# Optimization experiments

Hardware: AMD Instinct MI355X
Metric: run time of the kernel (lower is better)

## Reference

```python
import jax, jax.numpy as jnp
import numpy as np

B, S, H, E, TOPK = 8, 512, 1024, 8, 2


def setup_inputs() -> dict:
    key = jax.random.key(0)
    ks = jax.random.split(key, 10)
    D = 2 * H
    inp = {
        "vector": jax.random.normal(ks[0], (B, S, D), dtype=jnp.float32),
        # gate weights (Linear(H, E)): stored as [H, E] for x @ W + b
        "Wg": jax.random.normal(ks[1], (H, E), dtype=jnp.float32) * 0.02,
        "bg": jnp.zeros((E,), dtype=jnp.float32),
        "Wf": jax.random.normal(ks[2], (H, E), dtype=jnp.float32) * 0.02,
        "bf": jnp.zeros((E,), dtype=jnp.float32),
        # expert MLP weights, stacked over experts: Linear(2H,2H) -> ReLU -> Linear(2H,2H)
        "W1": jax.random.normal(ks[3], (E, D, D), dtype=jnp.float32) * 0.02,
        "b1": jnp.zeros((E, D), dtype=jnp.float32),
        "W2": jax.random.normal(ks[4], (E, D, D), dtype=jnp.float32) * 0.02,
        "b2": jnp.zeros((E, D), dtype=jnp.float32),
        # combine weights (config['initializer_weight'])
        "weight": jnp.ones((2,), dtype=jnp.float32),
        "top_k": TOPK,
    }
    return inp


def reference(vector, Wg, bg, Wf, bf, W1, b1, W2, b2, weight, top_k):
    h = Wg.shape[0]
    n_exp = Wg.shape[1]
    # gate_g on first half, softmax, then top-k sparsify (scatter of topk values)
    rout_g = jax.nn.softmax(vector[:, :, :h] @ Wg + bg, axis=-1)           # [B,S,E]
    vals, idx = jax.lax.top_k(rout_g, top_k)                               # [B,S,k]
    route_g = jnp.sum(jax.nn.one_hot(idx, n_exp, dtype=vals.dtype) * vals[..., None], axis=-2)  # [B,S,E]
    # gate_f on second half: dense softmax routing
    rout_f = jax.nn.softmax(vector[:, :, h:2 * h] @ Wf + bf, axis=-1)      # [B,S,E]
    # dense expert computation for every token (dropout = identity at eval)
    hidden = jax.nn.relu(jnp.einsum('bsd,edh->bseh', vector, W1) + b1)     # [B,S,E,2H]
    expert_out = jnp.einsum('bseh,ehd->bsed', hidden, W2) + b2             # [B,S,E,2H]
    out0 = weight[0] * jnp.einsum('bsed,bse->bsd', expert_out[..., :h], route_g)
    out1 = weight[1] * jnp.einsum('bsed,bse->bsd', expert_out[..., h:2 * h], rout_f)
    return (out0, out1)
```

## Files before the change

### kernel.cpp

```cpp
#include <hip/hip_runtime.h>

#define TOKENS 4096
#define DDIM   2048
#define HDIM   1024
#define NEXP   8
#define GK     2048
#define GN     2048

typedef __bf16 bf16_t;
typedef __bf16 bf16x8 __attribute__((ext_vector_type(8)));
typedef __bf16 bf16x4 __attribute__((ext_vector_type(4)));
typedef float  f32x4  __attribute__((ext_vector_type(4)));

__device__ inline void gld_lds16(const bf16_t* g, bf16_t* l) {
  __builtin_amdgcn_global_load_lds(
      (const __attribute__((address_space(1))) void*)g,
      (__attribute__((address_space(3))) void*)l, 16, 0, 0);
}

#define LGKM0() asm volatile("s_waitcnt lgkmcnt(0)" ::: "memory")
#define VMC(n)  asm volatile("s_waitcnt vmcnt(" #n ")" ::: "memory")
#define BAR()   __builtin_amdgcn_s_barrier()

__global__ __launch_bounds__(256)
void k_routing(const float* __restrict__ vec,
               const float* __restrict__ Wg, const float* __restrict__ bg,
               const float* __restrict__ Wf, const float* __restrict__ bfv,
               const float* __restrict__ wgt,
               float* __restrict__ c0, float* __restrict__ c1)
{
  const int wave = threadIdx.x >> 6;
  const int lane = threadIdx.x & 63;
  const int m = blockIdx.x * 4 + wave;
  const float* v = vec + (size_t)m * DDIM;

  float ag[NEXP], af[NEXP];
#pragma unroll
  for (int e = 0; e < NEXP; ++e) { ag[e] = 0.f; af[e] = 0.f; }

  for (int i = lane; i < HDIM; i += 64) {
    const float xg = v[i];
    const float xf = v[HDIM + i];
    const float4 wg0 = *(const float4*)(Wg + i * NEXP);
    const float4 wg1 = *(const float4*)(Wg + i * NEXP + 4);
    const float4 wf0 = *(const float4*)(Wf + i * NEXP);
    const float4 wf1 = *(const float4*)(Wf + i * NEXP + 4);
    ag[0] += xg * wg0.x; ag[1] += xg * wg0.y; ag[2] += xg * wg0.z; ag[3] += xg * wg0.w;
    ag[4] += xg * wg1.x; ag[5] += xg * wg1.y; ag[6] += xg * wg1.z; ag[7] += xg * wg1.w;
    af[0] += xf * wf0.x; af[1] += xf * wf0.y; af[2] += xf * wf0.z; af[3] += xf * wf0.w;
    af[4] += xf * wf1.x; af[5] += xf * wf1.y; af[6] += xf * wf1.z; af[7] += xf * wf1.w;
  }
#pragma unroll
  for (int e = 0; e < NEXP; ++e) {
#pragma unroll
    for (int off = 32; off >= 1; off >>= 1) {
      ag[e] += __shfl_xor(ag[e], off, 64);
      af[e] += __shfl_xor(af[e], off, 64);
    }
  }
  if (lane == 0) {
    float g[NEXP], f[NEXP];
    float mg = -1e30f, mf = -1e30f;
#pragma unroll
    for (int e = 0; e < NEXP; ++e) {
      g[e] = ag[e] + bg[e]; mg = fmaxf(mg, g[e]);
      f[e] = af[e] + bfv[e]; mf = fmaxf(mf, f[e]);
    }
    float sg = 0.f, sf = 0.f;
#pragma unroll
    for (int e = 0; e < NEXP; ++e) {
      g[e] = expf(g[e] - mg); sg += g[e];
      f[e] = expf(f[e] - mf); sf += f[e];
    }
    const float rg = 1.f / sg, rf = 1.f / sf;
#pragma unroll
    for (int e = 0; e < NEXP; ++e) { g[e] *= rg; f[e] *= rf; }
    int i1 = 0;
#pragma unroll
    for (int e = 1; e < NEXP; ++e) if (g[e] > g[i1]) i1 = e;
    int i2 = (i1 == 0) ? 1 : 0;
#pragma unroll
    for (int e = 0; e < NEXP; ++e) if (e != i1 && g[e] > g[i2]) i2 = e;
    const float w0 = wgt[0], w1 = wgt[1];
#pragma unroll
    for (int e = 0; e < NEXP; ++e) {
      c0[e * TOKENS + m] = (e == i1 || e == i2) ? w0 * g[e] : 0.f;
      c1[e * TOKENS + m] = w1 * f[e];
    }
  }
}

__global__ __launch_bounds__(256)
void k_cvt(const float* __restrict__ in, bf16_t* __restrict__ out)
{
  const size_t i = ((size_t)blockIdx.x * 256 + threadIdx.x) * 8;
  const float4 a = *(const float4*)(in + i);
  const float4 b = *(const float4*)(in + i + 4);
  bf16x8 o;
  o[0] = (bf16_t)a.x; o[1] = (bf16_t)a.y; o[2] = (bf16_t)a.z; o[3] = (bf16_t)a.w;
  o[4] = (bf16_t)b.x; o[5] = (bf16_t)b.y; o[6] = (bf16_t)b.z; o[7] = (bf16_t)b.w;
  *(bf16x8*)(out + i) = o;
}

#define TP 68
__global__ __launch_bounds__(256)
void k_cvt_wt(const float* __restrict__ W, bf16_t* __restrict__ Wt)
{
  __shared__ __attribute__((aligned(16))) bf16_t tile[64 * TP];
  const size_t eoff = (size_t)blockIdx.z * DDIM * DDIM;
  const float* w = W + eoff;
  bf16_t* wt = Wt + eoff;
  const int k0 = blockIdx.x * 64;
  const int n0 = blockIdx.y * 64;
  const int t = threadIdx.x;
  const int c4 = (t & 15) * 4;
  const int rb = (t >> 4) * 4;
#pragma unroll
  for (int rr = 0; rr < 4; ++rr) {
    const int r = rb + rr;
    const float4 v = *(const float4*)(w + (size_t)(k0 + r) * DDIM + n0 + c4);
    tile[(c4 + 0) * TP + r] = (bf16_t)v.x;
    tile[(c4 + 1) * TP + r] = (bf16_t)v.y;
    tile[(c4 + 2) * TP + r] = (bf16_t)v.z;
    tile[(c4 + 3) * TP + r] = (bf16_t)v.w;
  }
  __syncthreads();
  const int nl = t >> 2;
  const int kq = (t & 3) * 16;
  bf16_t* dst = wt + (size_t)(n0 + nl) * DDIM + k0 + kq;
#pragma unroll
  for (int j2 = 0; j2 < 4; ++j2) {
    bf16x4 u = *(const bf16x4*)(&tile[nl * TP + kq + j2 * 4]);
    *(bf16x4*)(dst + j2 * 4) = u;
  }
}


#define FRG(base, R, KQ) \
  (*(const bf16x8*)((base) + ((((R) * 32 + (KQ)) ^ ((((R) >> 3) & 1) << 4)))))

#define MFMA_(d, x, y) (d) = __builtin_amdgcn_mfma_f32_16x16x32_bf16((x), (y), (d), 0, 0, 0)

#define PHASE(U, PA, STA, STB, NP) do { \
    bf16x8 _a[8], _b0, _b1; \
    _Pragma("unroll") \
    for (int _i = 0; _i < 8; ++_i) _a[_i] = FRG(AsF + (U) * 8192, wm + _i * 16 + fr, kq); \
    _b0 = FRG(BsF + (U) * 4096, wn + fr, kq); \
    _b1 = FRG(BsF + (U) * 4096, wn + 16 + fr, kq); \
    if ((PA) < (NP)) { STA(PA, (PA) & 3); STB(PA, (PA) & 3); } \
    BAR(); LGKM0(); \
    __builtin_amdgcn_s_setprio(1); \
    _Pragma("unroll") \
    for (int _i = 0; _i < 8; ++_i) { MFMA_(acc[_i][0], _a[_i], _b0); MFMA_(acc[_i][1], _a[_i], _b1); } \
    __builtin_amdgcn_s_setprio(0); \
  } while (0)

#define TILE(U0, U1, PA, PB, STA, STB, NP) do { \
    PHASE(U0, PA, STA, STB, NP); \
    BAR(); \
    PHASE(U1, PB, STA, STB, NP); \
    if ((PB) < (NP)) { VMC(3); } else { VMC(0); } \
    BAR(); \
  } while (0)

__global__ __launch_bounds__(512, 2)
void k_gemm1_8p(const bf16_t* __restrict__ A, const bf16_t* __restrict__ W1t,
                const float* __restrict__ b1, bf16_t* __restrict__ Hd)
{
  __shared__ __attribute__((aligned(16))) bf16_t AsF[4 * 8192];
  __shared__ __attribute__((aligned(16))) bf16_t BsF[4 * 4096];
  const int e = blockIdx.z;
  const int t = threadIdx.x;
  const int wave = t >> 6, lane = t & 63;
  const int m0 = blockIdx.x * 256, n0 = blockIdx.y * 128;
  const int wm = (wave >> 2) * 128, wn = (wave & 3) * 32;
  const int fr = lane & 15, kq = (lane >> 4) * 8;

  const int sRw = wave * 16 + (lane >> 2);
  const int sC  = ((lane & 3) * 8) ^ (((lane >> 5) & 1) << 4);
  const bf16_t* aSrc = A + (size_t)(m0 + sRw) * GK + sC;
  const bf16_t* bSrc = W1t + (size_t)e * GN * GK + (size_t)(n0 + sRw) * GK + sC;
  bf16_t* aDst = AsF + wave * 512;
  bf16_t* bDst = BsF + wave * 512;

#define STA1(p, u) do { const bf16_t* _s = aSrc + (size_t)(p) * 32; \
    gld_lds16(_s, aDst + (u) * 8192); \
    gld_lds16(_s + (size_t)128 * GK, aDst + (u) * 8192 + 4096); } while (0)
#define STB1(p, u) gld_lds16(bSrc + (size_t)(p) * 32, bDst + (u) * 4096)

  f32x4 acc[8][2] = {};

  STA1(0, 0); STB1(0, 0);
  STA1(1, 1); STB1(1, 1);
  STA1(2, 2); STB1(2, 2);
  asm volatile("s_waitcnt vmcnt(3)" ::: "memory");
  BAR();

#pragma unroll 1
  for (int tt = 0; tt < 32; tt += 2) {
    TILE(0, 1, 2 * tt + 3, 2 * tt + 4, STA1, STB1, 64);
    TILE(2, 3, 2 * tt + 5, 2 * tt + 6, STA1, STB1, 64);
  }

  const float* bias = b1 + (size_t)e * DDIM;
  bf16_t* Hb = Hd + (size_t)e * TOKENS * DDIM;
  const int ecol = lane & 15, erow = (lane >> 4) * 4;
#pragma unroll
  for (int j = 0; j < 2; ++j) {
    const int gn = n0 + wn + j * 16 + ecol;
    const float bv = bias[gn];
#pragma unroll
    for (int i = 0; i < 8; ++i) {
      const int gm = m0 + wm + i * 16 + erow;
#pragma unroll
      for (int r = 0; r < 4; ++r) {
        float v = acc[i][j][r] + bv;
        v = v > 0.f ? v : 0.f;
        Hb[(size_t)(gm + r) * DDIM + gn] = (bf16_t)v;
      }
    }
  }
#undef STA1
#undef STB1
}

__global__ __launch_bounds__(512, 2)
void k_gemm2_8p(const bf16_t* __restrict__ Hd, const bf16_t* __restrict__ W2t,
                const float* __restrict__ b2,
                const float* __restrict__ c0, const float* __restrict__ c1,
                float* __restrict__ out0, float* __restrict__ out1)
{
  __shared__ __attribute__((aligned(16))) bf16_t AsF[4 * 8192];
  __shared__ __attribute__((aligned(16))) bf16_t BsF[4 * 4096];
  __shared__ float cs[NEXP][256];
  __shared__ float bsh[NEXP][128];

  const int t = threadIdx.x;
  const int wave = t >> 6, lane = t & 63;
  const int m0 = blockIdx.x * 256, n0 = blockIdx.y * 128;
  const int wm = (wave >> 2) * 128, wn = (wave & 3) * 32;
  const int fr = lane & 15, kq = (lane >> 4) * 8;
  const bool hi = (n0 >= HDIM);
  const float* cc = hi ? c1 : c0;

  for (int idx = t; idx < NEXP * 256; idx += 512) {
    const int ee = idx >> 8, r = idx & 255;
    cs[ee][r] = cc[ee * TOKENS + m0 + r];
  }
  for (int idx = t; idx < NEXP * 128; idx += 512) {
    const int ee = idx >> 7, r = idx & 127;
    bsh[ee][r] = b2[ee * DDIM + n0 + r];
  }

  const int sRw = wave * 16 + (lane >> 2);
  const int sC  = ((lane & 3) * 8) ^ (((lane >> 5) & 1) << 4);
  const bf16_t* aSrc = Hd + (size_t)(m0 + sRw) * GK + sC;
  const bf16_t* bSrc = W2t + (size_t)(n0 + sRw) * GK + sC;
  bf16_t* aDst = AsF + wave * 512;
  bf16_t* bDst = BsF + wave * 512;

#define STA2(p, u) do { \
    const bf16_t* _s = aSrc + (size_t)((p) >> 6) * ((size_t)TOKENS * GK) + (size_t)(((p) & 63) * 32); \
    gld_lds16(_s, aDst + (u) * 8192); \
    gld_lds16(_s + (size_t)128 * GK, aDst + (u) * 8192 + 4096); } while (0)
#define STB2(p, u) do { \
    const bf16_t* _s = bSrc + (size_t)((p) >> 6) * ((size_t)GN * GK) + (size_t)(((p) & 63) * 32); \
    gld_lds16(_s, bDst + (u) * 4096); } while (0)

  f32x4 acc[8][2] = {};
  f32x4 fin[8][2] = {};

  STA2(0, 0); STB2(0, 0);
  STA2(1, 1); STB2(1, 1);
  STA2(2, 2); STB2(2, 2);
  asm volatile("s_waitcnt vmcnt(3) lgkmcnt(0)" ::: "memory");
  BAR();

  const int ecol = lane & 15, erow = (lane >> 4) * 4;

#pragma unroll 1
  for (int ex = 0; ex < NEXP; ++ex) {
#pragma unroll 1
    for (int tt = 0; tt < 32; tt += 2) {
      const int gt = ex * 32 + tt;
      TILE(0, 1, 2 * gt + 3, 2 * gt + 4, STA2, STB2, 512);
      TILE(2, 3, 2 * gt + 5, 2 * gt + 6, STA2, STB2, 512);
    }
#pragma unroll
    for (int j = 0; j < 2; ++j) {
      const float bv = bsh[ex][wn + j * 16 + ecol];
#pragma unroll
      for (int i = 0; i < 8; ++i) {
        const int rw = wm + i * 16 + erow;
#pragma unroll
        for (int r = 0; r < 4; ++r) {
          fin[i][j][r] += cs[ex][rw + r] * (acc[i][j][r] + bv);
          acc[i][j][r] = 0.f;
        }
      }
    }
  }

#pragma unroll
  for (int j = 0; j < 2; ++j) {
    const int gn = n0 + wn + j * 16 + ecol;
    float* ob = hi ? (out1 + (gn - HDIM)) : (out0 + gn);
#pragma unroll
    for (int i = 0; i < 8; ++i) {
      const int gm = m0 + wm + i * 16 + erow;
#pragma unroll
      for (int r = 0; r < 4; ++r)
        ob[(size_t)(gm + r) * HDIM] = fin[i][j][r];
    }
  }
#undef STA2
#undef STB2
}

__global__ __launch_bounds__(256, 2)
void k_gemm_relu(const bf16_t* __restrict__ A, const bf16_t* __restrict__ W1t,
                 const float* __restrict__ b1, bf16_t* __restrict__ Hd)
{
  __shared__ __attribute__((aligned(16))) bf16_t As[128 * 32];
  __shared__ __attribute__((aligned(16))) bf16_t Bs[128 * 32];
  const int e = blockIdx.z;
  const bf16_t* Bt = W1t + (size_t)e * GK * GN;
  const float* bias = b1 + (size_t)e * GN;
  bf16_t* H = Hd + (size_t)e * TOKENS * GN;

  const int t = threadIdx.x;
  const int wave = t >> 6;
  const int lane = t & 63;
  const int m0 = blockIdx.x * 128;
  const int n0 = blockIdx.y * 128;
  const int wm = (wave >> 1) << 6;
  const int wn = (wave & 1) << 6;

  f32x4 acc[4][4] = {};

  const bf16_t* aP0 = A + (size_t)(m0 + (t >> 2)) * GK + (t & 3) * 8;
  const bf16_t* aP1 = aP0 + (size_t)64 * GK;
  const bf16_t* bP0 = Bt + (size_t)(n0 + (t >> 2)) * GK + (t & 3) * 8;
  const bf16_t* bP1 = bP0 + (size_t)64 * GK;
  bf16_t* lA0 = As + wave * 512;
  bf16_t* lA1 = As + 2048 + wave * 512;
  bf16_t* lB0 = Bs + wave * 512;
  bf16_t* lB1 = Bs + 2048 + wave * 512;

  const int fr = lane & 15;
  const int kq = (lane >> 4) * 8;

  for (int k0 = 0; k0 < GK; k0 += 32) {
    gld_lds16(aP0 + k0, lA0);
    gld_lds16(aP1 + k0, lA1);
    gld_lds16(bP0 + k0, lB0);
    gld_lds16(bP1 + k0, lB1);
    __syncthreads();
    bf16x8 afr[4], bfr[4];
#pragma unroll
    for (int i = 0; i < 4; ++i) {
      afr[i] = *(const bf16x8*)(As + (wm + i * 16 + fr) * 32 + kq);
      bfr[i] = *(const bf16x8*)(Bs + (wn + i * 16 + fr) * 32 + kq);
    }
#pragma unroll
    for (int i = 0; i < 4; ++i)
#pragma unroll
      for (int j = 0; j < 4; ++j)
        acc[i][j] = __builtin_amdgcn_mfma_f32_16x16x32_bf16(afr[i], bfr[j], acc[i][j], 0, 0, 0);
    __syncthreads();
  }

  const int col = lane & 15;
  const int rq  = (lane >> 4) * 4;
#pragma unroll
  for (int j = 0; j < 4; ++j) {
    const int gn = n0 + wn + j * 16 + col;
    const float bv = bias[gn];
#pragma unroll
    for (int i = 0; i < 4; ++i) {
      const int gm = m0 + wm + i * 16 + rq;
#pragma unroll
      for (int r = 0; r < 4; ++r) {
        float v = acc[i][j][r] + bv;
        v = v > 0.f ? v : 0.f;
        H[(size_t)(gm + r) * GN + gn] = (bf16_t)v;
      }
    }
  }
}

__global__ __launch_bounds__(256, 2)
void k_gemm_out(const bf16_t* __restrict__ A, const bf16_t* __restrict__ Bt,
                const float* __restrict__ bias,
                const float* __restrict__ c0, const float* __restrict__ c1,
                float* __restrict__ out0, float* __restrict__ out1, const int accum)
{
  __shared__ __attribute__((aligned(16))) bf16_t As[128 * 32];
  __shared__ __attribute__((aligned(16))) bf16_t Bs[128 * 32];
  const int t = threadIdx.x;
  const int wave = t >> 6;
  const int lane = t & 63;
  const int m0 = blockIdx.x * 128;
  const int n0 = blockIdx.y * 128;
  const int wm = (wave >> 1) << 6;
  const int wn = (wave & 1) << 6;

  f32x4 acc[4][4] = {};

  const bf16_t* aP0 = A + (size_t)(m0 + (t >> 2)) * GK + (t & 3) * 8;
  const bf16_t* aP1 = aP0 + (size_t)64 * GK;
  const bf16_t* bP0 = Bt + (size_t)(n0 + (t >> 2)) * GK + (t & 3) * 8;
  const bf16_t* bP1 = bP0 + (size_t)64 * GK;
  bf16_t* lA0 = As + wave * 512;
  bf16_t* lA1 = As + 2048 + wave * 512;
  bf16_t* lB0 = Bs + wave * 512;
  bf16_t* lB1 = Bs + 2048 + wave * 512;

  const int fr = lane & 15;
  const int kq = (lane >> 4) * 8;

  for (int k0 = 0; k0 < GK; k0 += 32) {
    gld_lds16(aP0 + k0, lA0);
    gld_lds16(aP1 + k0, lA1);
    gld_lds16(bP0 + k0, lB0);
    gld_lds16(bP1 + k0, lB1);
    __syncthreads();
    bf16x8 afr[4], bfr[4];
#pragma unroll
    for (int i = 0; i < 4; ++i) {
      afr[i] = *(const bf16x8*)(As + (wm + i * 16 + fr) * 32 + kq);
      bfr[i] = *(const bf16x8*)(Bs + (wn + i * 16 + fr) * 32 + kq);
    }
#pragma unroll
    for (int i = 0; i < 4; ++i)
#pragma unroll
      for (int j = 0; j < 4; ++j)
        acc[i][j] = __builtin_amdgcn_mfma_f32_16x16x32_bf16(afr[i], bfr[j], acc[i][j], 0, 0, 0);
    __syncthreads();
  }

  const int col = lane & 15;
  const int rq  = (lane >> 4) * 4;
#pragma unroll
  for (int j = 0; j < 4; ++j) {
    const int gn = n0 + wn + j * 16 + col;
    const float bv = bias[gn];
    const bool lo = gn < HDIM;
    float* obase = lo ? (out0 + gn) : (out1 + (gn - HDIM));
    const float* cc = lo ? c0 : c1;
#pragma unroll
    for (int i = 0; i < 4; ++i) {
      const int gmB = m0 + wm + i * 16 + rq;
#pragma unroll
      for (int r = 0; r < 4; ++r) {
        const int gm = gmB + r;
        float v = (acc[i][j][r] + bv) * cc[gm];
        float* dst = obase + (size_t)gm * HDIM;
        if (accum) v += *dst;
        *dst = v;
      }
    }
  }
}

extern "C" void kernel_launch(void* const* d_in, const int* in_sizes, int n_in,
                              void* d_out, int out_size, void* d_ws, size_t ws_size,
                              hipStream_t stream)
{
  const float* vec = (const float*)d_in[0];
  const float* Wg  = (const float*)d_in[1];
  const float* bg  = (const float*)d_in[2];
  const float* Wf  = (const float*)d_in[3];
  const float* bfv = (const float*)d_in[4];
  const float* W1  = (const float*)d_in[5];
  const float* b1  = (const float*)d_in[6];
  const float* W2  = (const float*)d_in[7];
  const float* b2  = (const float*)d_in[8];
  const float* wgt = (const float*)d_in[9];

  float* out0 = (float*)d_out;
  float* out1 = out0 + (size_t)TOKENS * HDIM;

  char* base = (char*)d_ws;
  const size_t XB = (size_t)TOKENS * DDIM * 2;
  const size_t HB = (size_t)NEXP * TOKENS * DDIM * 2;
  const size_t WT = (size_t)NEXP * DDIM * DDIM * 2;

  bf16_t* Xbf = (bf16_t*)base;
  float*  c0  = (float*)(base + XB);
  float*  c1  = c0 + (size_t)NEXP * TOKENS;
  size_t off = XB + 2 * (size_t)NEXP * TOKENS * 4;

  k_routing<<<dim3(TOKENS / 4), 256, 0, stream>>>(vec, Wg, bg, Wf, bfv, wgt, c0, c1);
  k_cvt<<<dim3((TOKENS * DDIM) / 2048), 256, 0, stream>>>(vec, Xbf);

  if (ws_size >= off + HB + 2 * WT) {
    bf16_t* hidden = (bf16_t*)(base + off);
    bf16_t* W1t    = (bf16_t*)(base + off + HB);
    bf16_t* W2t    = (bf16_t*)(base + off + HB + WT);
    k_cvt_wt<<<dim3(32, 32, NEXP), 256, 0, stream>>>(W1, W1t);
    k_cvt_wt<<<dim3(32, 32, NEXP), 256, 0, stream>>>(W2, W2t);
    k_gemm1_8p<<<dim3(16, 16, NEXP), 512, 0, stream>>>(Xbf, W1t, b1, hidden);
    k_gemm2_8p<<<dim3(16, 16), 512, 0, stream>>>(hidden, W2t, b2, c0, c1, out0, out1);
  } else {
    bf16_t* hidden = (bf16_t*)(base + off);
    bf16_t* W1t    = hidden + (size_t)TOKENS * DDIM;
    bf16_t* W2t    = W1t + (size_t)DDIM * DDIM;
    for (int e = 0; e < NEXP; ++e) {
      k_cvt_wt<<<dim3(32, 32, 1), 256, 0, stream>>>(W1 + (size_t)e * DDIM * DDIM, W1t);
      k_cvt_wt<<<dim3(32, 32, 1), 256, 0, stream>>>(W2 + (size_t)e * DDIM * DDIM, W2t);
      k_gemm_relu<<<dim3(32, 16, 1), 256, 0, stream>>>(Xbf, W1t, b1 + (size_t)e * DDIM, hidden);
      k_gemm_out<<<dim3(32, 16), 256, 0, stream>>>(
          hidden, W2t, b2 + (size_t)e * DDIM,
          c0 + (size_t)e * TOKENS, c1 + (size_t)e * TOKENS, out0, out1, e > 0);
    }
  }
}
```

Measured before the change: 1.049 ms.

## Enlarge GEMM tiles and switch to single-barrier 4-stage pipeline

GEMM1 moves from a 256x128 to a 256x256 block tile, with each wave computing 128x64. GEMM2 reshapes to 128x256 tiles and launches a 32x8 grid. Both kernels replace the two-barrier PHASE/TILE scheme with one barrier per k-step over a 4-buffer ring, with matching vmcnt waits. The aim is to raise MFMA work per LDS fragment load and cut barrier stalls. The cost is more LDS per block (GEMM1 now about 128KB), which may limit occupancy to one block per CU, plus more accumulator registers.

```diff
diff --git a/kernel.cpp b/kernel.cpp
--- a/kernel.cpp
+++ b/kernel.cpp
@@ -141,39 +141,17 @@
 
 #define MFMA_(d, x, y) (d) = __builtin_amdgcn_mfma_f32_16x16x32_bf16((x), (y), (d), 0, 0, 0)
 
-#define PHASE(U, PA, STA, STB, NP) do { \
-    bf16x8 _a[8], _b0, _b1; \
-    _Pragma("unroll") \
-    for (int _i = 0; _i < 8; ++_i) _a[_i] = FRG(AsF + (U) * 8192, wm + _i * 16 + fr, kq); \
-    _b0 = FRG(BsF + (U) * 4096, wn + fr, kq); \
-    _b1 = FRG(BsF + (U) * 4096, wn + 16 + fr, kq); \
-    if ((PA) < (NP)) { STA(PA, (PA) & 3); STB(PA, (PA) & 3); } \
-    BAR(); LGKM0(); \
-    __builtin_amdgcn_s_setprio(1); \
-    _Pragma("unroll") \
-    for (int _i = 0; _i < 8; ++_i) { MFMA_(acc[_i][0], _a[_i], _b0); MFMA_(acc[_i][1], _a[_i], _b1); } \
-    __builtin_amdgcn_s_setprio(0); \
-  } while (0)
-
-#define TILE(U0, U1, PA, PB, STA, STB, NP) do { \
-    PHASE(U0, PA, STA, STB, NP); \
-    BAR(); \
-    PHASE(U1, PB, STA, STB, NP); \
-    if ((PB) < (NP)) { VMC(3); } else { VMC(0); } \
-    BAR(); \
-  } while (0)
-
 __global__ __launch_bounds__(512, 2)
 void k_gemm1_8p(const bf16_t* __restrict__ A, const bf16_t* __restrict__ W1t,
                 const float* __restrict__ b1, bf16_t* __restrict__ Hd)
 {
   __shared__ __attribute__((aligned(16))) bf16_t AsF[4 * 8192];
-  __shared__ __attribute__((aligned(16))) bf16_t BsF[4 * 4096];
+  __shared__ __attribute__((aligned(16))) bf16_t BsF[4 * 8192];
   const int e = blockIdx.z;
   const int t = threadIdx.x;
   const int wave = t >> 6, lane = t & 63;
-  const int m0 = blockIdx.x * 256, n0 = blockIdx.y * 128;
-  const int wm = (wave >> 2) * 128, wn = (wave & 3) * 32;
+  const int m0 = blockIdx.x * 256, n0 = blockIdx.y * 256;
+  const int wm = (wave >> 2) * 128, wn = (wave & 3) * 64;
   const int fr = lane & 15, kq = (lane >> 4) * 8;
 
   const int sRw = wave * 16 + (lane >> 2);
@@ -183,30 +161,53 @@
   bf16_t* aDst = AsF + wave * 512;
   bf16_t* bDst = BsF + wave * 512;
 
-#define STA1(p, u) do { const bf16_t* _s = aSrc + (size_t)(p) * 32; \
-    gld_lds16(_s, aDst + (u) * 8192); \
-    gld_lds16(_s + (size_t)128 * GK, aDst + (u) * 8192 + 4096); } while (0)
-#define STB1(p, u) gld_lds16(bSrc + (size_t)(p) * 32, bDst + (u) * 4096)
-
-  f32x4 acc[8][2] = {};
+#define STA1(P, U) do { const bf16_t* _s = aSrc + (size_t)(P) * 32; \
+    gld_lds16(_s, aDst + (U) * 8192); \
+    gld_lds16(_s + (size_t)128 * GK, aDst + (U) * 8192 + 4096); } while (0)
+#define STB1(P, U) do { const bf16_t* _s = bSrc + (size_t)(P) * 32; \
+    gld_lds16(_s, bDst + (U) * 8192); \
+    gld_lds16(_s + (size_t)128 * GK, bDst + (U) * 8192 + 4096); } while (0)
+
+  f32x4 acc[8][4] = {};
+
+#define PH1(U, SP, SU, DOST) do { \
+    bf16x8 a_[8], b_[4]; \
+    _Pragma("unroll") \
+    for (int _i = 0; _i < 8; ++_i) a_[_i] = FRG(AsF + (U) * 8192, wm + _i * 16 + fr, kq); \
+    _Pragma("unroll") \
+    for (int _j = 0; _j < 4; ++_j) b_[_j] = FRG(BsF + (U) * 8192, wn + _j * 16 + fr, kq); \
+    if (DOST) { STA1(SP, SU); STB1(SP, SU); } \
+    LGKM0(); \
+    __builtin_amdgcn_s_setprio(1); \
+    _Pragma("unroll") \
+    for (int _i = 0; _i < 8; ++_i) \
+      _Pragma("unroll") \
+      for (int _j = 0; _j < 4; ++_j) MFMA_(acc[_i][_j], a_[_i], b_[_j]); \
+    __builtin_amdgcn_s_setprio(0); \
+  } while (0)
 
   STA1(0, 0); STB1(0, 0);
   STA1(1, 1); STB1(1, 1);
   STA1(2, 2); STB1(2, 2);
-  asm volatile("s_waitcnt vmcnt(3)" ::: "memory");
-  BAR();
+  VMC(8); BAR();
 
 #pragma unroll 1
-  for (int tt = 0; tt < 32; tt += 2) {
-    TILE(0, 1, 2 * tt + 3, 2 * tt + 4, STA1, STB1, 64);
-    TILE(2, 3, 2 * tt + 5, 2 * tt + 6, STA1, STB1, 64);
-  }
+  for (int pb = 0; pb < 60; pb += 4) {
+    PH1(0, pb + 3, 3, 1); VMC(8); BAR();
+    PH1(1, pb + 4, 0, 1); VMC(8); BAR();
+    PH1(2, pb + 5, 1, 1); VMC(8); BAR();
+    PH1(3, pb + 6, 2, 1); VMC(8); BAR();
+  }
+  PH1(0, 63, 3, 1); VMC(8); BAR();
+  PH1(1, 0, 0, 0);  VMC(4); BAR();
+  PH1(2, 0, 0, 0);  VMC(0); BAR();
+  PH1(3, 0, 0, 0);
 
   const float* bias = b1 + (size_t)e * DDIM;
   bf16_t* Hb = Hd + (size_t)e * TOKENS * DDIM;
   const int ecol = lane & 15, erow = (lane >> 4) * 4;
 #pragma unroll
-  for (int j = 0; j < 2; ++j) {
+  for (int j = 0; j < 4; ++j) {
     const int gn = n0 + wn + j * 16 + ecol;
     const float bv = bias[gn];
 #pragma unroll
@@ -220,6 +221,7 @@
       }
     }
   }
+#undef PH1
 #undef STA1
 #undef STB1
 }
@@ -230,27 +232,28 @@
                 const float* __restrict__ c0, const float* __restrict__ c1,
                 float* __restrict__ out0, float* __restrict__ out1)
 {
-  __shared__ __attribute__((aligned(16))) bf16_t AsF[4 * 8192];
-  __shared__ __attribute__((aligned(16))) bf16_t BsF[4 * 4096];
-  __shared__ float cs[NEXP][256];
-  __shared__ float bsh[NEXP][128];
+  __shared__ __attribute__((aligned(16))) bf16_t AsF[4 * 4096];
+  __shared__ __attribute__((aligned(16))) bf16_t BsF[4 * 8192];
+  __shared__ float cs[NEXP][128];
+  __shared__ float bsh[NEXP][256];
 
   const int t = threadIdx.x;
   const int wave = t >> 6, lane = t & 63;
-  const int m0 = blockIdx.x * 256, n0 = blockIdx.y * 128;
-  const int wm = (wave >> 2) * 128, wn = (wave & 3) * 32;
+  const int m0 = blockIdx.x * 128, n0 = blockIdx.y * 256;
+  const int wm = (wave >> 2) * 64, wn = (wave & 3) * 64;
   const int fr = lane & 15, kq = (lane >> 4) * 8;
   const bool hi = (n0 >= HDIM);
   const float* cc = hi ? c1 : c0;
 
+  for (int idx = t; idx < NEXP * 128; idx += 512) {
+    const int ee = idx >> 7, r = idx & 127;
+    cs[ee][r] = cc[ee * TOKENS + m0 + r];
+  }
   for (int idx = t; idx < NEXP * 256; idx += 512) {
     const int ee = idx >> 8, r = idx & 255;
-    cs[ee][r] = cc[ee * TOKENS + m0 + r];
-  }
-  for (int idx = t; idx < NEXP * 128; idx += 512) {
-    const int ee = idx >> 7, r = idx & 127;
     bsh[ee][r] = b2[ee * DDIM + n0 + r];
   }
+  __syncthreads();
 
   const int sRw = wave * 16 + (lane >> 2);
   const int sC  = ((lane & 3) * 8) ^ (((lane >> 5) & 1) << 4);
@@ -259,62 +262,87 @@
   bf16_t* aDst = AsF + wave * 512;
   bf16_t* bDst = BsF + wave * 512;
 
-#define STA2(p, u) do { \
-    const bf16_t* _s = aSrc + (size_t)((p) >> 6) * ((size_t)TOKENS * GK) + (size_t)(((p) & 63) * 32); \
-    gld_lds16(_s, aDst + (u) * 8192); \
-    gld_lds16(_s + (size_t)128 * GK, aDst + (u) * 8192 + 4096); } while (0)
-#define STB2(p, u) do { \
-    const bf16_t* _s = bSrc + (size_t)((p) >> 6) * ((size_t)GN * GK) + (size_t)(((p) & 63) * 32); \
-    gld_lds16(_s, bDst + (u) * 4096); } while (0)
-
-  f32x4 acc[8][2] = {};
-  f32x4 fin[8][2] = {};
+#define STA2(P, U) do { \
+    const bf16_t* _s = aSrc + (size_t)((P) >> 6) * ((size_t)TOKENS * GK) + (size_t)((P) & 63) * 32; \
+    gld_lds16(_s, aDst + (U) * 4096); } while (0)
+#define STB2(P, U) do { \
+    const bf16_t* _s = bSrc + (size_t)((P) >> 6) * ((size_t)GN * GK) + (size_t)((P) & 63) * 32; \
+    gld_lds16(_s, bDst + (U) * 8192); \
+    gld_lds16(_s + (size_t)128 * GK, bDst + (U) * 8192 + 4096); } while (0)
+
+  f32x4 acc[4][4] = {};
+  f32x4 fin[4][4] = {};
+
+#define PH2(U, SP, SU, DOST) do { \
+    bf16x8 a_[4], b_[4]; \
+    _Pragma("unroll") \
+    for (int _i = 0; _i < 4; ++_i) a_[_i] = FRG(AsF + (U) * 4096, wm + _i * 16 + fr, kq); \
+    _Pragma("unroll") \
+    for (int _j = 0; _j < 4; ++_j) b_[_j] = FRG(BsF + (U) * 8192, wn + _j * 16 + fr, kq); \
+    if (DOST) { STA2(SP, SU); STB2(SP, SU); } \
+    LGKM0(); \
+    __builtin_amdgcn_s_setprio(1); \
+    _Pragma("unroll") \
+    for (int _i = 0; _i < 4; ++_i) \
+      _Pragma("unroll") \
+      for (int _j = 0; _j < 4; ++_j) MFMA_(acc[_i][_j], a_[_i], b_[_j]); \
+    __builtin_amdgcn_s_setprio(0); \
+  } while (0)
+
+  const int ecol = lane & 15, erow = (lane >> 4) * 4;
+
+#define FOLD2(E) do { \
+    _Pragma("unroll") \
+    for (int _j = 0; _j < 4; ++_j) { \
+      const float _bv = bsh[E][wn + _j * 16 + ecol]; \
+      _Pragma("unroll") \
+      for (int _i = 0; _i < 4; ++_i) { \
+        const int _rw = wm + _i * 16 + erow; \
+        _Pragma("unroll") \
+        for (int _r = 0; _r < 4; ++_r) { \
+          fin[_i][_j][_r] += cs[E][_rw + _r] * (acc[_i][_j][_r] + _bv); \
+          acc[_i][_j][_r] = 0.f; \
+        } \
+      } \
+    } \
+  } while (0)
 
   STA2(0, 0); STB2(0, 0);
   STA2(1, 1); STB2(1, 1);
   STA2(2, 2); STB2(2, 2);
-  asm volatile("s_waitcnt vmcnt(3) lgkmcnt(0)" ::: "memory");
-  BAR();
-
-  const int ecol = lane & 15, erow = (lane >> 4) * 4;
+  VMC(6); BAR();
 
 #pragma unroll 1
-  for (int ex = 0; ex < NEXP; ++ex) {
-#pragma unroll 1
-    for (int tt = 0; tt < 32; tt += 2) {
-      const int gt = ex * 32 + tt;
-      TILE(0, 1, 2 * gt + 3, 2 * gt + 4, STA2, STB2, 512);
-      TILE(2, 3, 2 * gt + 5, 2 * gt + 6, STA2, STB2, 512);
-    }
-#pragma unroll
-    for (int j = 0; j < 2; ++j) {
-      const float bv = bsh[ex][wn + j * 16 + ecol];
-#pragma unroll
-      for (int i = 0; i < 8; ++i) {
-        const int rw = wm + i * 16 + erow;
-#pragma unroll
-        for (int r = 0; r < 4; ++r) {
-          fin[i][j][r] += cs[ex][rw + r] * (acc[i][j][r] + bv);
-          acc[i][j][r] = 0.f;
-        }
-      }
-    }
-  }
-
-#pragma unroll
-  for (int j = 0; j < 2; ++j) {
+  for (int pb = 0; pb < 508; pb += 4) {
+    PH2(0, pb + 3, 3, 1); VMC(6); BAR();
+    PH2(1, pb + 4, 0, 1); VMC(6); BAR();
+    PH2(2, pb + 5, 1, 1); VMC(6); BAR();
+    PH2(3, pb + 6, 2, 1);
+    if ((pb & 63) == 60) FOLD2((pb + 3) >> 6);
+    VMC(6); BAR();
+  }
+  PH2(0, 511, 3, 1); VMC(6); BAR();
+  PH2(1, 0, 0, 0);  VMC(3); BAR();
+  PH2(2, 0, 0, 0);  VMC(0); BAR();
+  PH2(3, 0, 0, 0);
+  FOLD2(7);
+
+#pragma unroll
+  for (int j = 0; j < 4; ++j) {
     const int gn = n0 + wn + j * 16 + ecol;
     float* ob = hi ? (out1 + (gn - HDIM)) : (out0 + gn);
 #pragma unroll
-    for (int i = 0; i < 8; ++i) {
+    for (int i = 0; i < 4; ++i) {
       const int gm = m0 + wm + i * 16 + erow;
 #pragma unroll
       for (int r = 0; r < 4; ++r)
         ob[(size_t)(gm + r) * HDIM] = fin[i][j][r];
     }
   }
+#undef PH2
 #undef STA2
 #undef STB2
+#undef FOLD2
 }
 
 __global__ __launch_bounds__(256, 2)
@@ -500,8 +528,8 @@
     bf16_t* W2t    = (bf16_t*)(base + off + HB + WT);
     k_cvt_wt<<<dim3(32, 32, NEXP), 256, 0, stream>>>(W1, W1t);
     k_cvt_wt<<<dim3(32, 32, NEXP), 256, 0, stream>>>(W2, W2t);
-    k_gemm1_8p<<<dim3(16, 16, NEXP), 512, 0, stream>>>(Xbf, W1t, b1, hidden);
-    k_gemm2_8p<<<dim3(16, 16), 512, 0, stream>>>(hidden, W2t, b2, c0, c1, out0, out1);
+    k_gemm1_8p<<<dim3(16, 8, NEXP), 512, 0, stream>>>(Xbf, W1t, b1, hidden);
+    k_gemm2_8p<<<dim3(32, 8), 512, 0, stream>>>(hidden, W2t, b2, c0, c1, out0, out1);
   } else {
     bf16_t* hidden = (bf16_t*)(base + off);
     bf16_t* W1t    = hidden + (size_t)TOKENS * DDIM;
```

Result: faster. 956.5 us (-8.8%).
